# Optimization experiments

Measured on AMD Instinct MI355X. Metric: run time of the kernel, lower is better.

Reference implementation:

```python
import jax, jax.numpy as jnp
import numpy as np

MARGIN = 0.3
NORM_EPS = 1e-12  # torch F.normalize default eps


def setup_inputs() -> dict:
    key = jax.random.key(0)
    k1, k2 = jax.random.split(key)
    embeddings = jax.random.normal(k1, (8192, 128), dtype=jnp.float32)
    labels = jax.random.randint(k2, (8192,), 0, 128, dtype=jnp.int64)
    return {"embeddings": embeddings, "labels": labels}


def _triplet_loss(embeddings, labels):
    # L2-normalize rows (torch F.normalize: x / max(||x||, eps))
    norm = jnp.linalg.norm(embeddings, axis=1, keepdims=True)
    e = embeddings / jnp.maximum(norm, NORM_EPS)

    # pairwise squared Euclidean via gram matrix
    dot = e @ e.T                     # [B, B]
    sq = jnp.diagonal(dot)            # [B]
    d2 = jnp.clip(sq[None, :] - 2.0 * dot + sq[:, None], 0.0)
    zmask = (d2 == 0.0).astype(d2.dtype)
    dist = jnp.sqrt(d2 + zmask * 1e-16) * (1.0 - zmask)  # [B, B]

    # hard mining, fully vectorized over rows
    same = labels[:, None] == labels[None, :]
    eye = jnp.eye(labels.shape[0], dtype=bool)
    pos_mask = same & ~eye
    neg_mask = ~same

    dist_ap = jnp.max(jnp.where(pos_mask, dist, -jnp.inf), axis=1)  # hardest positive
    dist_an = jnp.min(jnp.where(neg_mask, dist, jnp.inf), axis=1)   # hardest negative

    valid = pos_mask.any(axis=1) & neg_mask.any(axis=1)
    # MarginRankingLoss(margin)(dist_an, dist_ap, y=1) = mean relu(dist_ap - dist_an + margin)
    per_row = jnp.maximum(dist_ap - dist_an + MARGIN, 0.0)
    n_valid = jnp.maximum(jnp.sum(valid), 1).astype(dist.dtype)
    loss = jnp.sum(jnp.where(valid, per_row, 0.0)) / n_valid
    return jnp.where(valid.any(), loss, jnp.zeros((), dist.dtype))


def reference(embeddings, labels):
    return _triplet_loss(embeddings, labels)
```

## Files before the change

### kernel.cpp

```cpp
#include <hip/hip_runtime.h>
#include <cmath>

#define BN 8192
#define DIM 128
#define MARGIN_F 0.3f
#define NSPLIT 8
#define CPS 1024
#define NT 8
#define NPART (NSPLIT * 2)
#define FBLK 32
#define IMAX 0x7FFFFFFF
#define IMIN 0x80000000

typedef __attribute__((ext_vector_type(4))) int i32x4;

__device__ __forceinline__ int imin3(int a, int b, int c) { return min(a, min(b, c)); }
__device__ __forceinline__ int imax3(int a, int b, int c) { return max(a, max(b, c)); }

__global__ __launch_bounds__(256) void norm_cvt_k(
    const float* __restrict__ emb, const int* __restrict__ lab,
    float* __restrict__ sqv, unsigned short* __restrict__ EnQ16,
    unsigned* __restrict__ LP)
{
  int gt = blockIdx.x * blockDim.x + threadIdx.x;
  if (gt < 2048) {
    int base = (gt >> 4) * 64 + (gt & 15);
    LP[gt] = (unsigned)(lab[base] & 255) | ((unsigned)(lab[base + 16] & 255) << 8) |
             ((unsigned)(lab[base + 32] & 255) << 16) | ((unsigned)(lab[base + 48] & 255) << 24);
  }

  int w = gt >> 6;
  int lane = threadIdx.x & 63;
  if (w >= BN) return;
  float2 v = *reinterpret_cast<const float2*>(&emb[w * DIM + lane * 2]);
  float s = v.x * v.x + v.y * v.y;
  #pragma unroll
  for (int off = 32; off > 0; off >>= 1) s += __shfl_xor(s, off);
  float iv = 1.0f / fmaxf(sqrtf(s), 1e-12f);
  if (lane == 0) sqv[w] = s * iv * iv;
  int q0 = (int)rintf(127.0f * v.x * iv);
  int q1 = (int)rintf(127.0f * v.y * iv);
  unsigned short us = (unsigned short)((q0 & 255) | ((q1 & 255) << 8));
  int g = lane >> 3;
  EnQ16[(g * BN + w) * 8 + (lane & 7)] = us;
}

__global__ __launch_bounds__(256, 2) void gram_mine_mfma_k(
    const char* __restrict__ EnQ, const int* __restrict__ lab,
    const unsigned* __restrict__ LP,
    int* __restrict__ ap_part, int* __restrict__ an_part)
{
  const int tid = threadIdx.x;
  const int w = tid >> 6, l = tid & 63;
  const int wr = w >> 1, wc = w & 1;
  const int lrow = l & 15, lkg = l >> 4;

  const int rowBase = blockIdx.x * 128 + wr * 64;
  const int panel   = blockIdx.y * CPS;

  i32x4 a[4][2];
  #pragma unroll
  for (int mi = 0; mi < 4; ++mi)
    #pragma unroll
    for (int kk = 0; kk < 2; ++kk)
      a[mi][kk] = *reinterpret_cast<const i32x4*>(
          EnQ + (((size_t)((kk << 2) + lkg) * BN + rowBase + mi * 16 + lrow) << 4));

  int rlv[4][4];
  #pragma unroll
  for (int mi = 0; mi < 4; ++mi) {
    int rb = rowBase + mi * 16 + lkg * 4;
    #pragma unroll
    for (int r = 0; r < 4; ++r) rlv[mi][r] = lab[rb + r] & 255;
  }

  int ap[4][4], an[4][4];
  #pragma unroll
  for (int mi = 0; mi < 4; ++mi)
    #pragma unroll
    for (int r = 0; r < 4; ++r) { ap[mi][r] = IMAX; an[mi][r] = IMIN; }

  const i32x4 zf = {0, 0, 0, 0};

  const int colLane = wc * 64 + lrow;
  const char* bp0 = EnQ + (((size_t)lkg * BN + panel + colLane) << 4);
  const char* bp1 = bp0 + ((size_t)BN << 6);

  auto loadHalf = [&](i32x4 (&b)[2][2], const char* p0, const char* p1, int n0) {
    #pragma unroll
    for (int n = 0; n < 2; ++n) {
      b[0][n] = *reinterpret_cast<const i32x4*>(p0 + (n0 + n) * 256);
      b[1][n] = *reinterpret_cast<const i32x4*>(p1 + (n0 + n) * 256);
    }
  };
  auto mfmaHalf = [&](i32x4 (&A)[4][2], const i32x4 (&b)[2][2]) {
    #pragma unroll
    for (int mi = 0; mi < 4; ++mi)
      #pragma unroll
      for (int n = 0; n < 2; ++n)
        A[mi][n] = __builtin_amdgcn_mfma_i32_16x16x64_i8(a[mi][0], b[0][n], zf, 0, 0, 0);
    #pragma unroll
    for (int mi = 0; mi < 4; ++mi)
      #pragma unroll
      for (int n = 0; n < 2; ++n)
        A[mi][n] = __builtin_amdgcn_mfma_i32_16x16x64_i8(a[mi][1], b[1][n], A[mi][n], 0, 0, 0);
  };

  auto mineTile = [&](const i32x4 (&A)[4][2], int l0, int l1, int c0, int c1, bool dg) {
    if (!dg) {
      #pragma unroll
      for (int mi = 0; mi < 4; ++mi)
        #pragma unroll
        for (int r = 0; r < 4; ++r) {
          int d0 = A[mi][0][r], d1 = A[mi][1][r];
          bool s0 = (rlv[mi][r] == l0), s1 = (rlv[mi][r] == l1);
          int p0 = s0 ? d0 : IMAX;
          int p1 = s1 ? d1 : IMAX;
          int q0 = s0 ? IMIN : d0;
          int q1 = s1 ? IMIN : d1;
          ap[mi][r] = imin3(ap[mi][r], p0, p1);
          an[mi][r] = imax3(an[mi][r], q0, q1);
        }
    } else {
      #pragma unroll
      for (int mi = 0; mi < 4; ++mi)
        #pragma unroll
        for (int r = 0; r < 4; ++r) {
          int rloc = mi * 16 + lkg * 4 + r;
          int d0 = A[mi][0][r], d1 = A[mi][1][r];
          bool s0 = (rlv[mi][r] == l0), s1 = (rlv[mi][r] == l1);
          bool e0 = (rloc == c0), e1 = (rloc == c1);
          int p0 = (s0 && !e0) ? d0 : IMAX;
          int p1 = (s1 && !e1) ? d1 : IMAX;
          int q0 = s0 ? IMIN : d0;
          int q1 = s1 ? IMIN : d1;
          ap[mi][r] = imin3(ap[mi][r], p0, p1);
          an[mi][r] = imax3(an[mi][r], q0, q1);
        }
    }
  };

  i32x4 accA[4][2], accB[4][2];
  i32x4 bA[2][2], bB[2][2];
  int lprev0 = 0, lprev1 = 0;
  bool diagP = false;

  loadHalf(bA, bp0, bp1, 0);

  #pragma unroll 1
  for (int ct = 0; ct < NT; ++ct) {
    const int colBase = panel + ct * 128 + wc * 64;
    const bool diag = (rowBase == colBase);

    const unsigned LPv = LP[(colBase >> 6) * 16 + lrow];
    const int l0 = (int)(LPv & 255u),         l1 = (int)((LPv >> 8) & 255u);
    const int l2 = (int)((LPv >> 16) & 255u), l3 = (int)(LPv >> 24);

    loadHalf(bB, bp0, bp1, 2);
    mfmaHalf(accA, bA);
    if (ct > 0) mineTile(accB, lprev0, lprev1, 32 + lrow, 48 + lrow, diagP);

    bp0 += 2048; bp1 += 2048;
    if (ct + 1 < NT) loadHalf(bA, bp0, bp1, 0);

    mfmaHalf(accB, bB);
    mineTile(accA, l0, l1, 0 + lrow, 16 + lrow, diag);

    lprev0 = l2; lprev1 = l3; diagP = diag;
  }
  mineTile(accB, lprev0, lprev1, 32 + lrow, 48 + lrow, diagP);

  const int part = blockIdx.y * 2 + wc;
  #pragma unroll
  for (int mi = 0; mi < 4; ++mi)
    #pragma unroll
    for (int r = 0; r < 4; ++r) {
      int p = ap[mi][r], n = an[mi][r];
      #pragma unroll
      for (int off = 1; off < 16; off <<= 1) {
        p = min(p, __shfl_xor(p, off));
        n = max(n, __shfl_xor(n, off));
      }
      if (lrow == 0) {
        int rg = rowBase + mi * 16 + lkg * 4 + r;
        ap_part[part * BN + rg] = p;
        an_part[part * BN + rg] = n;
      }
    }
}

__global__ __launch_bounds__(256) void finalize_a_k(
    const int* __restrict__ ap_part, const int* __restrict__ an_part,
    const float* __restrict__ sqv,
    float* __restrict__ blk_sum, float* __restrict__ blk_cnt)
{
  int r = blockIdx.x * 256 + threadIdx.x;
  int apt = IMAX, ant = IMIN;
  #pragma unroll 8
  for (int s = 0; s < NPART; ++s) {
    apt = min(apt, ap_part[s * BN + r]);
    ant = max(ant, an_part[s * BN + r]);
  }
  float sum = 0.f, cnt = 0.f;
  if (apt != IMAX && ant != IMIN) {
    const float sc = 2.0f / (127.0f * 127.0f);
    float rs1 = sqv[r] + 1.0f;
    float dap = sqrtf(fmaxf(fmaf(-sc, (float)apt, rs1), 0.f));
    float dan = sqrtf(fmaxf(fmaf(-sc, (float)ant, rs1), 0.f));
    sum = fmaxf(dap - dan + MARGIN_F, 0.f);
    cnt = 1.f;
  }
  #pragma unroll
  for (int off = 32; off > 0; off >>= 1) {
    sum += __shfl_xor(sum, off);
    cnt += __shfl_xor(cnt, off);
  }
  __shared__ float ssum[4], scnt[4];
  int wv = threadIdx.x >> 6;
  if ((threadIdx.x & 63) == 0) { ssum[wv] = sum; scnt[wv] = cnt; }
  __syncthreads();
  if (threadIdx.x == 0) {
    blk_sum[blockIdx.x] = ssum[0] + ssum[1] + ssum[2] + ssum[3];
    blk_cnt[blockIdx.x] = scnt[0] + scnt[1] + scnt[2] + scnt[3];
  }
}

__global__ __launch_bounds__(64) void finalize_b_k(
    const float* __restrict__ blk_sum, const float* __restrict__ blk_cnt,
    float* __restrict__ out)
{
  int l = threadIdx.x;
  float s = (l < FBLK) ? blk_sum[l] : 0.f;
  float c = (l < FBLK) ? blk_cnt[l] : 0.f;
  #pragma unroll
  for (int off = 32; off > 0; off >>= 1) {
    s += __shfl_xor(s, off);
    c += __shfl_xor(c, off);
  }
  if (l == 0) out[0] = (c > 0.f) ? (s / c) : 0.f;
}

extern "C" void kernel_launch(void* const* d_in, const int* in_sizes, int n_in,
                              void* d_out, int out_size, void* d_ws, size_t ws_size,
                              hipStream_t stream)
{
  const float* emb = (const float*)d_in[0];
  const int*   lab = (const int*)d_in[1];
  float* out = (float*)d_out;
  float* ws  = (float*)d_ws;

  float*    sqv     = ws;
  int*      ap_part = (int*)(sqv + BN);
  int*      an_part = ap_part + NPART * BN;
  float*    blk_sum = (float*)(an_part + NPART * BN);
  float*    blk_cnt = blk_sum + FBLK;
  unsigned* LP      = (unsigned*)(blk_cnt + FBLK);
  char*     EnQ     = (char*)(LP + 2048);

  norm_cvt_k<<<dim3(BN / 4), 256, 0, stream>>>(emb, lab, sqv, (unsigned short*)EnQ, LP);
  gram_mine_mfma_k<<<dim3(BN / 128, NSPLIT), 256, 0, stream>>>(EnQ, lab, LP, ap_part, an_part);
  finalize_a_k<<<dim3(FBLK), 256, 0, stream>>>(ap_part, an_part, sqv, blk_sum, blk_cnt);
  finalize_b_k<<<dim3(1), 64, 0, stream>>>(blk_sum, blk_cnt, out);
}
```

Measured before the change: 33.26 us.

## Counting-sort rows by label so most tiles skip positive-mask mining

Adds a single-block histogram and prefix-scan kernel, then scatters the normalized quantized rows into label-sorted order with atomics. Each 64-row group records its label range, so column tiles whose range cannot overlap the row tile's range use a cheap max-only mining path with no label compares. This cuts the per-element VALU cost in the mining epilogue. In exchange it adds an extra serial launch, atomic scatter with nondeterministic order, and uncoalesced label-range loads.

```diff
diff --git a/kernel.cpp b/kernel.cpp
--- a/kernel.cpp
+++ b/kernel.cpp
@@ -9,6 +9,7 @@
 #define NT 8
 #define NPART (NSPLIT * 2)
 #define FBLK 32
+#define NLAB 128
 #define IMAX 0x7FFFFFFF
 #define IMIN 0x80000000
 
@@ -17,37 +18,68 @@
 __device__ __forceinline__ int imin3(int a, int b, int c) { return min(a, min(b, c)); }
 __device__ __forceinline__ int imax3(int a, int b, int c) { return max(a, max(b, c)); }
 
+__global__ __launch_bounds__(256) void sort_prep_k(
+    const int* __restrict__ lab, int* __restrict__ binCur, int* __restrict__ LR)
+{
+  __shared__ int h[NLAB];
+  __shared__ int incl[NLAB];
+  const int t = threadIdx.x;
+  if (t < NLAB) h[t] = 0;
+  __syncthreads();
+  for (int i = t; i < BN; i += 256) atomicAdd(&h[lab[i] & (NLAB - 1)], 1);
+  __syncthreads();
+  if (t < NLAB) incl[t] = h[t];
+  __syncthreads();
+  #pragma unroll
+  for (int off = 1; off < NLAB; off <<= 1) {
+    int v = (t < NLAB && t >= off) ? incl[t - off] : 0;
+    __syncthreads();
+    if (t < NLAB) incl[t] += v;
+    __syncthreads();
+  }
+  if (t < NLAB) {
+    binCur[t] = incl[t] - h[t];
+    int p0 = t * 64, p1 = t * 64 + 63;
+    int lo = 0, hi = NLAB - 1;
+    while (lo < hi) { int m = (lo + hi) >> 1; if (incl[m] > p0) hi = m; else lo = m + 1; }
+    int lab0 = lo;
+    lo = lab0; hi = NLAB - 1;
+    while (lo < hi) { int m = (lo + hi) >> 1; if (incl[m] > p1) hi = m; else lo = m + 1; }
+    LR[t] = lab0 | (lo << 8);
+  }
+}
+
 __global__ __launch_bounds__(256) void norm_cvt_k(
     const float* __restrict__ emb, const int* __restrict__ lab,
-    float* __restrict__ sqv, unsigned short* __restrict__ EnQ16,
-    unsigned* __restrict__ LP)
+    float* __restrict__ sqvS, unsigned short* __restrict__ EnQ16,
+    int* __restrict__ labS, int* __restrict__ binCur)
 {
   int gt = blockIdx.x * blockDim.x + threadIdx.x;
-  if (gt < 2048) {
-    int base = (gt >> 4) * 64 + (gt & 15);
-    LP[gt] = (unsigned)(lab[base] & 255) | ((unsigned)(lab[base + 16] & 255) << 8) |
-             ((unsigned)(lab[base + 32] & 255) << 16) | ((unsigned)(lab[base + 48] & 255) << 24);
-  }
-
   int w = gt >> 6;
   int lane = threadIdx.x & 63;
   if (w >= BN) return;
+
+  int lb = 0, dst = 0;
+  if (lane == 0) { lb = lab[w] & (NLAB - 1); dst = atomicAdd(&binCur[lb], 1); }
+  dst = __shfl(dst, 0);
+  lb  = __shfl(lb, 0);
+
   float2 v = *reinterpret_cast<const float2*>(&emb[w * DIM + lane * 2]);
   float s = v.x * v.x + v.y * v.y;
   #pragma unroll
   for (int off = 32; off > 0; off >>= 1) s += __shfl_xor(s, off);
   float iv = 1.0f / fmaxf(sqrtf(s), 1e-12f);
-  if (lane == 0) sqv[w] = s * iv * iv;
+  if (lane == 0) { sqvS[dst] = s * iv * iv; labS[dst] = lb; }
   int q0 = (int)rintf(127.0f * v.x * iv);
   int q1 = (int)rintf(127.0f * v.y * iv);
   unsigned short us = (unsigned short)((q0 & 255) | ((q1 & 255) << 8));
   int g = lane >> 3;
-  EnQ16[(g * BN + w) * 8 + (lane & 7)] = us;
+  EnQ16[(g * BN + dst) * 8 + (lane & 7)] = us;
 }
 
 __global__ __launch_bounds__(256, 2) void gram_mine_mfma_k(
-    const char* __restrict__ EnQ, const int* __restrict__ lab,
-    const unsigned* __restrict__ LP,
+    const char* __restrict__ EnQ, const int* __restrict__ labS,
+    const int* __restrict__ LR,
     int* __restrict__ ap_part, int* __restrict__ an_part)
 {
   const int tid = threadIdx.x;
@@ -58,6 +90,9 @@
   const int rowBase = blockIdx.x * 128 + wr * 64;
   const int panel   = blockIdx.y * CPS;
 
+  const int LRr = LR[rowBase >> 6];
+  const int rLo = LRr & 255, rHi = (LRr >> 8) & 255;
+
   i32x4 a[4][2];
   #pragma unroll
   for (int mi = 0; mi < 4; ++mi)
@@ -71,7 +106,7 @@
   for (int mi = 0; mi < 4; ++mi) {
     int rb = rowBase + mi * 16 + lkg * 4;
     #pragma unroll
-    for (int r = 0; r < 4; ++r) rlv[mi][r] = lab[rb + r] & 255;
+    for (int r = 0; r < 4; ++r) rlv[mi][r] = labS[rb + r];
   }
 
   int ap[4][4], an[4][4];
@@ -106,7 +141,14 @@
         A[mi][n] = __builtin_amdgcn_mfma_i32_16x16x64_i8(a[mi][1], b[1][n], A[mi][n], 0, 0, 0);
   };
 
-  auto mineTile = [&](const i32x4 (&A)[4][2], int l0, int l1, int c0, int c1, bool dg) {
+  auto mineFast = [&](const i32x4 (&A)[4][2]) {
+    #pragma unroll
+    for (int mi = 0; mi < 4; ++mi)
+      #pragma unroll
+      for (int r = 0; r < 4; ++r)
+        an[mi][r] = imax3(an[mi][r], A[mi][0][r], A[mi][1][r]);
+  };
+  auto mineMixed = [&](const i32x4 (&A)[4][2], int l0, int l1, int c0, int c1, bool dg) {
     if (!dg) {
       #pragma unroll
       for (int mi = 0; mi < 4; ++mi)
@@ -142,33 +184,43 @@
 
   i32x4 accA[4][2], accB[4][2];
   i32x4 bA[2][2], bB[2][2];
-  int lprev0 = 0, lprev1 = 0;
-  bool diagP = false;
+  int lp0 = 0, lp1 = 0;
+  bool diagP = false, mixedP = false;
 
   loadHalf(bA, bp0, bp1, 0);
 
   #pragma unroll 1
   for (int ct = 0; ct < NT; ++ct) {
     const int colBase = panel + ct * 128 + wc * 64;
-    const bool diag = (rowBase == colBase);
-
-    const unsigned LPv = LP[(colBase >> 6) * 16 + lrow];
-    const int l0 = (int)(LPv & 255u),         l1 = (int)((LPv >> 8) & 255u);
-    const int l2 = (int)((LPv >> 16) & 255u), l3 = (int)(LPv >> 24);
+    const int LRc = LR[colBase >> 6];
+    const int cLo = LRc & 255, cHi = (LRc >> 8) & 255;
+    const bool mixed = (cHi >= rLo) && (cLo <= rHi);
+    const bool diag  = (rowBase == colBase);
+
+    int l0 = 0, l1 = 0, l2 = 0, l3 = 0;
+    if (mixed) {
+      l0 = labS[colBase + lrow];       l1 = labS[colBase + 16 + lrow];
+      l2 = labS[colBase + 32 + lrow];  l3 = labS[colBase + 48 + lrow];
+    }
 
     loadHalf(bB, bp0, bp1, 2);
     mfmaHalf(accA, bA);
-    if (ct > 0) mineTile(accB, lprev0, lprev1, 32 + lrow, 48 + lrow, diagP);
+    if (ct > 0) {
+      if (mixedP) mineMixed(accB, lp0, lp1, 32 + lrow, 48 + lrow, diagP);
+      else        mineFast(accB);
+    }
 
     bp0 += 2048; bp1 += 2048;
     if (ct + 1 < NT) loadHalf(bA, bp0, bp1, 0);
 
     mfmaHalf(accB, bB);
-    mineTile(accA, l0, l1, 0 + lrow, 16 + lrow, diag);
-
-    lprev0 = l2; lprev1 = l3; diagP = diag;
-  }
-  mineTile(accB, lprev0, lprev1, 32 + lrow, 48 + lrow, diagP);
+    if (mixed) mineMixed(accA, l0, l1, 0 + lrow, 16 + lrow, diag);
+    else       mineFast(accA);
+
+    lp0 = l2; lp1 = l3; diagP = diag; mixedP = mixed;
+  }
+  if (mixedP) mineMixed(accB, lp0, lp1, 32 + lrow, 48 + lrow, diagP);
+  else        mineFast(accB);
 
   const int part = blockIdx.y * 2 + wc;
   #pragma unroll
@@ -191,7 +243,7 @@
 
 __global__ __launch_bounds__(256) void finalize_a_k(
     const int* __restrict__ ap_part, const int* __restrict__ an_part,
-    const float* __restrict__ sqv,
+    const float* __restrict__ sqvS,
     float* __restrict__ blk_sum, float* __restrict__ blk_cnt)
 {
   int r = blockIdx.x * 256 + threadIdx.x;
@@ -204,7 +256,7 @@
   float sum = 0.f, cnt = 0.f;
   if (apt != IMAX && ant != IMIN) {
     const float sc = 2.0f / (127.0f * 127.0f);
-    float rs1 = sqv[r] + 1.0f;
+    float rs1 = sqvS[r] + 1.0f;
     float dap = sqrtf(fmaxf(fmaf(-sc, (float)apt, rs1), 0.f));
     float dan = sqrtf(fmaxf(fmaf(-sc, (float)ant, rs1), 0.f));
     sum = fmaxf(dap - dan + MARGIN_F, 0.f);
@@ -249,16 +301,21 @@
   float* out = (float*)d_out;
   float* ws  = (float*)d_ws;
 
-  float*    sqv     = ws;
-  int*      ap_part = (int*)(sqv + BN);
-  int*      an_part = ap_part + NPART * BN;
-  float*    blk_sum = (float*)(an_part + NPART * BN);
-  float*    blk_cnt = blk_sum + FBLK;
-  unsigned* LP      = (unsigned*)(blk_cnt + FBLK);
-  char*     EnQ     = (char*)(LP + 2048);
-
-  norm_cvt_k<<<dim3(BN / 4), 256, 0, stream>>>(emb, lab, sqv, (unsigned short*)EnQ, LP);
-  gram_mine_mfma_k<<<dim3(BN / 128, NSPLIT), 256, 0, stream>>>(EnQ, lab, LP, ap_part, an_part);
-  finalize_a_k<<<dim3(FBLK), 256, 0, stream>>>(ap_part, an_part, sqv, blk_sum, blk_cnt);
+  float* sqvS     = ws;
+  int*   ap_part  = (int*)(sqvS + BN);
+  int*   an_part  = ap_part + NPART * BN;
+  float* blk_sum  = (float*)(an_part + NPART * BN);
+  float* blk_cnt  = blk_sum + FBLK;
+  int*   labS     = (int*)(blk_cnt + FBLK);
+  int*   binCur   = labS + BN;
+  int*   LR       = binCur + NLAB;
+  char*  EnQ      = (char*)(LR + NLAB + 16);
+
+  sort_prep_k<<<dim3(1), 256, 0, stream>>>(lab, binCur, LR);
+  norm_cvt_k<<<dim3(BN / 4), 256, 0, stream>>>(emb, lab, sqvS, (unsigned short*)EnQ,
+                                               labS, binCur);
+  gram_mine_mfma_k<<<dim3(BN / 128, NSPLIT), 256, 0, stream>>>(EnQ, labS, LR,
+                                                               ap_part, an_part);
+  finalize_a_k<<<dim3(FBLK), 256, 0, stream>>>(ap_part, an_part, sqvS, blk_sum, blk_cnt);
   finalize_b_k<<<dim3(1), 64, 0, stream>>>(blk_sum, blk_cnt, out);
 }
```

After: 51.34 us. 54.3% more time.
